# Performance work log

Hardware: AMD Instinct MI355X
Metric: run time of the kernel (lower is better)

Reference implementation:

```python
import jax, jax.numpy as jnp
import numpy as np

NUM_HEADS = 8
CHUNK = 64
TOP_K = 5


def setup_inputs() -> dict:
    key = jax.random.key(0)
    ks = jax.random.split(key, 5)
    D = 512
    x = jax.random.normal(ks[0], (1, 2048, D), dtype=jnp.float32)
    s = 0.02
    Wq = jax.random.normal(ks[1], (D, D), dtype=jnp.float32) * s
    Wk = jax.random.normal(ks[2], (D, D), dtype=jnp.float32) * s
    Wv = jax.random.normal(ks[3], (D, D), dtype=jnp.float32) * s
    Wo = jax.random.normal(ks[4], (D, D), dtype=jnp.float32) * s
    return {"x": x, "Wq": Wq, "Wk": Wk, "Wv": Wv, "Wo": Wo}


def reference(x, Wq, Wk, Wv, Wo):
    B, S, D = x.shape
    H = NUM_HEADS
    hd = D // H
    scale = hd ** -0.5
    C = S // CHUNK  # number of chunks

    def split_heads(t):
        return t.reshape(B, S, H, hd).transpose(0, 2, 1, 3)  # [B,H,S,hd]

    Q = split_heads(x @ Wq)
    K = split_heads(x @ Wk)
    V = split_heads(x @ Wv)

    # chunked K/V: [B,H,C,chunk,hd]
    Kc = K.reshape(B, H, C, CHUNK, hd)
    Vc = V.reshape(B, H, C, CHUNK, hd)

    # chunk descriptors: mean-pooled keys per chunk -> [B,H,C,hd]
    chunk_keys = Kc.mean(axis=3)

    # route each query to top-k chunks by scaled similarity
    sims = jnp.einsum('bhsd,bhcd->bhsc', Q, chunk_keys) * scale  # [B,H,S,C]
    _, idx = jax.lax.top_k(sims, TOP_K)  # [B,H,S,K]

    # gather selected K/V chunk blocks: [B,H,S,K,chunk,hd]
    idx_flat = idx.reshape(B, H, S * TOP_K)[:, :, :, None, None]
    Kg = jnp.take_along_axis(Kc, idx_flat, axis=2).reshape(B, H, S, TOP_K, CHUNK, hd)
    Vg = jnp.take_along_axis(Vc, idx_flat, axis=2).reshape(B, H, S, TOP_K, CHUNK, hd)

    # sparse block attention over the K*chunk gathered keys per query
    scores = jnp.einsum('bhsd,bhskcd->bhskc', Q, Kg) * scale
    attn = jax.nn.softmax(scores.reshape(B, H, S, TOP_K * CHUNK), axis=-1)
    attn = attn.reshape(B, H, S, TOP_K, CHUNK)
    out = jnp.einsum('bhskc,bhskcd->bhsd', attn, Vg)  # [B,H,S,hd]

    out = out.transpose(0, 2, 1, 3).reshape(B, S, D)
    return out @ Wo
```

## Files before the change

kernel.cpp:

```cpp
#include <hip/hip_runtime.h>
#include <hip/hip_bf16.h>
#include <math.h>

#define S_LEN 2048
#define D_DIM 512
#define H_NUM 8
#define HD    64
#define C_NUM 32
#define TOPK  5
#define SCALE 0.125f
#define QCAP  1024
#define ATILES 16

typedef __attribute__((ext_vector_type(8))) short bf16x8;
typedef __attribute__((ext_vector_type(4))) float f32x4;

__device__ __forceinline__ unsigned short f2b(float f) {
    __hip_bfloat16 h = __float2bfloat16(f);
    unsigned short u;
    __builtin_memcpy(&u, &h, 2);
    return u;
}
__device__ __forceinline__ bf16x8 pack8(float4 a, float4 b) {
    bf16x8 r;
    r[0] = (short)f2b(a.x); r[1] = (short)f2b(a.y);
    r[2] = (short)f2b(a.z); r[3] = (short)f2b(a.w);
    r[4] = (short)f2b(b.x); r[5] = (short)f2b(b.y);
    r[6] = (short)f2b(b.z); r[7] = (short)f2b(b.w);
    return r;
}
__device__ __forceinline__ float b2f(unsigned short u) {
    __hip_bfloat16 h;
    __builtin_memcpy(&h, &u, 2);
    return __bfloat162float(h);
}

#define BM 64
#define BN 64
#define BK 32

__device__ __forceinline__ void gemm_body(const float* __restrict__ A,
                                          const float* __restrict__ B,
                                          float* __restrict__ C,
                                          int M, int N, int K,
                                          int bx, int by) {
    __shared__ float As[BK][BM + 4];
    __shared__ float Bs[BK][BN];

    const int t  = threadIdx.x;
    const int tx = t & 15;
    const int ty = t >> 4;
    const int m0 = by * BM;
    const int n0 = bx * BN;

    float4 acc0 = make_float4(0.f,0.f,0.f,0.f);
    float4 acc1 = make_float4(0.f,0.f,0.f,0.f);
    float4 acc2 = make_float4(0.f,0.f,0.f,0.f);
    float4 acc3 = make_float4(0.f,0.f,0.f,0.f);

    const int ar = t >> 3;
    const int ac = (t & 7) * 4;
    const int br = t >> 4;
    const int bc = (t & 15) * 4;

    float4 a0, a1, b0, b1;
    auto LD = [&](int k0) {
        a0 = *(const float4*)&A[(size_t)(m0 + ar)      * K + k0 + ac];
        a1 = *(const float4*)&A[(size_t)(m0 + ar + 32) * K + k0 + ac];
        b0 = *(const float4*)&B[(size_t)(k0 + br)      * N + n0 + bc];
        b1 = *(const float4*)&B[(size_t)(k0 + br + 16) * N + n0 + bc];
    };

    LD(0);
    for (int k0 = 0; k0 < K; k0 += BK) {
        __syncthreads();
        As[ac+0][ar]    = a0.x; As[ac+1][ar]    = a0.y; As[ac+2][ar]    = a0.z; As[ac+3][ar]    = a0.w;
        As[ac+0][ar+32] = a1.x; As[ac+1][ar+32] = a1.y; As[ac+2][ar+32] = a1.z; As[ac+3][ar+32] = a1.w;
        *(float4*)&Bs[br][bc]      = b0;
        *(float4*)&Bs[br + 16][bc] = b1;
        __syncthreads();

        if (k0 + BK < K) LD(k0 + BK);

        #pragma unroll
        for (int kk = 0; kk < BK; ++kk) {
            float4 a = *(const float4*)&As[kk][ty * 4];
            float4 b = *(const float4*)&Bs[kk][tx * 4];
            acc0.x += a.x*b.x; acc0.y += a.x*b.y; acc0.z += a.x*b.z; acc0.w += a.x*b.w;
            acc1.x += a.y*b.x; acc1.y += a.y*b.y; acc1.z += a.y*b.z; acc1.w += a.y*b.w;
            acc2.x += a.z*b.x; acc2.y += a.z*b.y; acc2.z += a.z*b.z; acc2.w += a.z*b.w;
            acc3.x += a.w*b.x; acc3.y += a.w*b.y; acc3.z += a.w*b.z; acc3.w += a.w*b.w;
        }
    }

    *(float4*)&C[(size_t)(m0 + ty*4 + 0) * N + n0 + tx*4] = acc0;
    *(float4*)&C[(size_t)(m0 + ty*4 + 1) * N + n0 + tx*4] = acc1;
    *(float4*)&C[(size_t)(m0 + ty*4 + 2) * N + n0 + tx*4] = acc2;
    *(float4*)&C[(size_t)(m0 + ty*4 + 3) * N + n0 + tx*4] = acc3;
}

__device__ __forceinline__ void gemm_v_body(const float* __restrict__ A,
                                            const float* __restrict__ B,
                                            unsigned short* __restrict__ C,
                                            int M, int N, int K,
                                            int bx, int by) {
    __shared__ unsigned short Asv[64][72];
    __shared__ unsigned short Bsv[64][72];

    const int t  = threadIdx.x;
    const int m0 = by * 64;
    const int n0 = bx * 64;
    const int rl = t >> 2;
    const int c4 = (t & 3) * 16;

    const int lane = t & 63, w = t >> 6, lr = lane & 15, quad = lane >> 4;

    f32x4 acc[4] = {{0.f,0.f,0.f,0.f},{0.f,0.f,0.f,0.f},
                    {0.f,0.f,0.f,0.f},{0.f,0.f,0.f,0.f}};

    float4 fa[4], fb[4];
    auto LDA = [&](int k0) {
        const float* p = &A[(size_t)(m0 + rl) * K + k0 + c4];
        fa[0] = *(const float4*)&p[0];  fa[1] = *(const float4*)&p[4];
        fa[2] = *(const float4*)&p[8];  fa[3] = *(const float4*)&p[12];
    };
    auto LDB = [&](int k0) {
        const float* p = &B[(size_t)(k0 + rl) * N + n0 + c4];
        fb[0] = *(const float4*)&p[0];  fb[1] = *(const float4*)&p[4];
        fb[2] = *(const float4*)&p[8];  fb[3] = *(const float4*)&p[12];
    };

    LDA(0); LDB(0);
    for (int k0 = 0; k0 < K; k0 += 64) {
        __syncthreads();
        *(bf16x8*)&Asv[rl][c4]     = pack8(fa[0], fa[1]);
        *(bf16x8*)&Asv[rl][c4 + 8] = pack8(fa[2], fa[3]);
        #pragma unroll
        for (int f = 0; f < 4; ++f) {
            float4 v = fb[f];
            Bsv[c4 + f*4 + 0][rl] = f2b(v.x);
            Bsv[c4 + f*4 + 1][rl] = f2b(v.y);
            Bsv[c4 + f*4 + 2][rl] = f2b(v.z);
            Bsv[c4 + f*4 + 3][rl] = f2b(v.w);
        }
        __syncthreads();

        if (k0 + 64 < K) { LDA(k0 + 64); LDB(k0 + 64); }

        bf16x8 a0 = *(const bf16x8*)&Asv[w * 16 + lr][quad * 8];
        bf16x8 a1 = *(const bf16x8*)&Asv[w * 16 + lr][32 + quad * 8];
        #pragma unroll
        for (int nt = 0; nt < 4; ++nt) {
            bf16x8 b0 = *(const bf16x8*)&Bsv[nt * 16 + lr][quad * 8];
            bf16x8 b1 = *(const bf16x8*)&Bsv[nt * 16 + lr][32 + quad * 8];
            acc[nt] = __builtin_amdgcn_mfma_f32_16x16x32_bf16(a0, b0, acc[nt], 0, 0, 0);
            acc[nt] = __builtin_amdgcn_mfma_f32_16x16x32_bf16(a1, b1, acc[nt], 0, 0, 0);
        }
    }

    #pragma unroll
    for (int nt = 0; nt < 4; ++nt)
        #pragma unroll
        for (int r = 0; r < 4; ++r) {
            int m = m0 + w * 16 + quad * 4 + r;
            int n = n0 + nt * 16 + lr;
            C[(size_t)m * N + n] = f2b(acc[nt][r]);
        }
}

__global__ __launch_bounds__(256) void gemm_qkvz(const float* __restrict__ x,
                                                 const float* __restrict__ Wq,
                                                 const float* __restrict__ Wk,
                                                 const float* __restrict__ Wv,
                                                 float* __restrict__ Qb,
                                                 float* __restrict__ Kb,
                                                 unsigned short* __restrict__ Vbf,
                                                 int* __restrict__ cur) {
    if (blockIdx.z == 2) {
        if (blockIdx.x == 0 && blockIdx.y == 0) cur[threadIdx.x] = 0;
        gemm_v_body(x, Wv, Vbf, S_LEN, D_DIM, D_DIM, blockIdx.x, blockIdx.y);
    } else {
        const float* B = (blockIdx.z == 0) ? Wq : Wk;
        float*       C = (blockIdx.z == 0) ? Qb : Kb;
        gemm_body(x, B, C, S_LEN, D_DIM, D_DIM, blockIdx.x, blockIdx.y);
    }
}

__global__ __launch_bounds__(256) void chunk_keys_kernel(const float* __restrict__ K,
                                                         float* __restrict__ ck) {
    int i = blockIdx.x * 256 + threadIdx.x;
    int c = i >> 9;
    int d = i & 511;
    const float* p = K + (size_t)c * 64 * D_DIM + d;
    float sum = 0.f;
    #pragma unroll
    for (int r = 0; r < 64; ++r) sum += p[(size_t)r * D_DIM];
    ck[(size_t)c * D_DIM + d] = sum * (1.0f / 64.0f);
}

__global__ __launch_bounds__(256) void sims_topk(const float* __restrict__ Q,
                                                 const float* __restrict__ ck,
                                                 int* __restrict__ cur,
                                                 unsigned short* __restrict__ qlist) {
    __shared__ float qtile[64][68];
    __shared__ float cks[32][68];
    __shared__ float simsb[64][36];
    __shared__ int   lds_cnt[32];
    __shared__ int   lds_base[32];

    const int t  = threadIdx.x;
    const int s0 = blockIdx.x * 64;
    const int h  = blockIdx.y;

    if (t < 32) lds_cnt[t] = 0;

    {
        int r = t >> 2;
        #pragma unroll
        for (int i = 0; i < 4; ++i) {
            int cf4 = (t & 3) * 4 + i;
            *(float4*)&qtile[r][cf4 * 4] =
                *(const float4*)&Q[(size_t)(s0 + r) * D_DIM + h * HD + cf4 * 4];
        }
    }
    for (int i = t; i < C_NUM * 16; i += 256) {
        int c = i >> 4, df4 = i & 15;
        *(float4*)&cks[c][df4 * 4] =
            *(const float4*)&ck[(size_t)c * D_DIM + h * HD + df4 * 4];
    }
    __syncthreads();

    {
        const int sl = t >> 2, g = t & 3;
        float sa[8] = {0.f,0.f,0.f,0.f,0.f,0.f,0.f,0.f};
        #pragma unroll
        for (int d4 = 0; d4 < 16; ++d4) {
            float4 q4 = *(const float4*)&qtile[sl][d4 * 4];
            #pragma unroll
            for (int j = 0; j < 8; ++j) {
                float4 c4 = *(const float4*)&cks[g * 8 + j][d4 * 4];
                sa[j] += q4.x*c4.x + q4.y*c4.y + q4.z*c4.z + q4.w*c4.w;
            }
        }
        *(float4*)&simsb[sl][g*8 + 0] = make_float4(sa[0], sa[1], sa[2], sa[3]);
        *(float4*)&simsb[sl][g*8 + 4] = make_float4(sa[4], sa[5], sa[6], sa[7]);
    }
    __syncthreads();

    int csel[TOPK], lpos[TOPK];
    if (t < 64) {
        float sv[32];
        #pragma unroll
        for (int cq = 0; cq < 8; ++cq) {
            float4 v = *(const float4*)&simsb[t][cq * 4];
            sv[cq*4+0] = v.x; sv[cq*4+1] = v.y; sv[cq*4+2] = v.z; sv[cq*4+3] = v.w;
        }
        #pragma unroll
        for (int k = 0; k < TOPK; ++k) {
            float best = -INFINITY; int bi = 0;
            #pragma unroll
            for (int cc = 0; cc < 32; ++cc) {
                bool gt = sv[cc] > best;
                best = gt ? sv[cc] : best;
                bi   = gt ? cc : bi;
            }
            #pragma unroll
            for (int cc = 0; cc < 32; ++cc)
                if (cc == bi) sv[cc] = -INFINITY;
            csel[k] = bi;
            lpos[k] = atomicAdd(&lds_cnt[bi], 1);
        }
    }
    __syncthreads();

    if (t < 32) lds_base[t] = atomicAdd(&cur[h * 32 + t], lds_cnt[t]);
    __syncthreads();

    if (t < 64) {
        #pragma unroll
        for (int k = 0; k < TOPK; ++k) {
            int c = csel[k];
            int pos = lds_base[c] + lpos[k];
            if (pos < QCAP)
                qlist[(size_t)(h * 32 + c) * QCAP + pos] =
                    (unsigned short)((s0 + t) | (k << 11));
        }
    }
}

__global__ __launch_bounds__(256) void moc_attn6(const float* __restrict__ Q,
                                                 const float* __restrict__ K,
                                                 const unsigned short* __restrict__ Vbf,
                                                 const int* __restrict__ cnt,
                                                 const unsigned short* __restrict__ qlist,
                                                 float* __restrict__ lpart,
                                                 float* __restrict__ Opart) {
    __shared__ unsigned short Qs[64][72];
    __shared__ unsigned short Ks[64][72];
    __shared__ unsigned short VT[64][72];
    __shared__ unsigned short Ps[64][72];
    __shared__ unsigned short slist[64];

    const int hc = blockIdx.y;
    const int h  = hc >> 5;
    const int c  = hc & 31;
    const int g  = blockIdx.x;
    const int t  = threadIdx.x;

    const int count = min(cnt[hc], QCAP);
    const int base  = g * 64;
    if (base >= count) return;
    const int lim = min(count - base, 64);

    const float* Kb = K + ((size_t)c * 64) * D_DIM + h * HD;
    const unsigned short* Vb = Vbf + ((size_t)c * 64) * D_DIM + h * HD;
    const unsigned short* list = qlist + (size_t)hc * QCAP + base;

    {
        const int j  = t >> 2;
        const int d0 = (t & 3) * 16;

        const float* kr = Kb + (size_t)j * D_DIM + d0;
        float4 k0 = *(const float4*)&kr[0],  k1 = *(const float4*)&kr[4];
        float4 k2 = *(const float4*)&kr[8],  k3 = *(const float4*)&kr[12];
        *(bf16x8*)&Ks[j][d0]     = pack8(k0, k1);
        *(bf16x8*)&Ks[j][d0 + 8] = pack8(k2, k3);

        const unsigned short* vr = Vb + (size_t)j * D_DIM + d0;
        bf16x8 v0 = *(const bf16x8*)&vr[0];
        bf16x8 v1 = *(const bf16x8*)&vr[8];
        #pragma unroll
        for (int i = 0; i < 8; ++i) {
            VT[d0 + i][j]     = (unsigned short)v0[i];
            VT[d0 + 8 + i][j] = (unsigned short)v1[i];
        }

        unsigned short pv = (j < lim) ? list[j] : (unsigned short)0xFFFF;
        if ((t & 3) == 0) slist[j] = pv;
        int s = (pv == 0xFFFF) ? 0 : (int)(pv & 2047);
        const float* qr = Q + (size_t)s * D_DIM + h * HD + d0;
        float4 q0 = *(const float4*)&qr[0],  q1 = *(const float4*)&qr[4];
        float4 q2 = *(const float4*)&qr[8],  q3 = *(const float4*)&qr[12];
        *(bf16x8*)&Qs[j][d0]     = pack8(q0, q1);
        *(bf16x8*)&Qs[j][d0 + 8] = pack8(q2, q3);
    }
    __syncthreads();

    const int lane = t & 63;
    const int w    = t >> 6;
    const int lr   = lane & 15;
    const int quad = lane >> 4;

    bf16x8 aq0 = *(const bf16x8*)&Qs[w * 16 + lr][quad * 8];
    bf16x8 aq1 = *(const bf16x8*)&Qs[w * 16 + lr][32 + quad * 8];

    f32x4 acc[4];
    #pragma unroll
    for (int kt = 0; kt < 4; ++kt) {
        bf16x8 b0 = *(const bf16x8*)&Ks[kt * 16 + lr][quad * 8];
        bf16x8 b1 = *(const bf16x8*)&Ks[kt * 16 + lr][32 + quad * 8];
        f32x4 z = {0.f, 0.f, 0.f, 0.f};
        z = __builtin_amdgcn_mfma_f32_16x16x32_bf16(aq0, b0, z, 0, 0, 0);
        z = __builtin_amdgcn_mfma_f32_16x16x32_bf16(aq1, b1, z, 0, 0, 0);
        acc[kt] = z;
    }

    unsigned short pb[4][4];
    float dsum[4] = {0.f, 0.f, 0.f, 0.f};
    #pragma unroll
    for (int kt = 0; kt < 4; ++kt) {
        #pragma unroll
        for (int r = 0; r < 4; ++r) {
            unsigned short u = f2b(__expf(acc[kt][r] * SCALE));
            pb[kt][r] = u;
            dsum[r] += b2f(u);
        }
    }
    #pragma unroll
    for (int r = 0; r < 4; ++r) {
        float v = dsum[r];
        v += __shfl_xor(v, 1, 64);
        v += __shfl_xor(v, 2, 64);
        v += __shfl_xor(v, 4, 64);
        v += __shfl_xor(v, 8, 64);
        dsum[r] = v;
    }
    if (lr == 0) {
        #pragma unroll
        for (int r = 0; r < 4; ++r) {
            unsigned short sv = slist[w * 16 + quad * 4 + r];
            if (sv != 0xFFFF) {
                int kk = sv >> 11, s = sv & 2047;
                lpart[((size_t)kk * H_NUM + h) * S_LEN + s] = dsum[r];
            }
        }
    }

    #pragma unroll
    for (int kt = 0; kt < 4; ++kt)
        #pragma unroll
        for (int r = 0; r < 4; ++r)
            Ps[w * 16 + quad * 4 + r][kt * 16 + lr] = pb[kt][r];

    bf16x8 ap0 = *(const bf16x8*)&Ps[w * 16 + lr][quad * 8];
    bf16x8 ap1 = *(const bf16x8*)&Ps[w * 16 + lr][32 + quad * 8];

    #pragma unroll
    for (int dt = 0; dt < 4; ++dt) {
        bf16x8 b0 = *(const bf16x8*)&VT[dt * 16 + lr][quad * 8];
        bf16x8 b1 = *(const bf16x8*)&VT[dt * 16 + lr][32 + quad * 8];
        f32x4 z = {0.f, 0.f, 0.f, 0.f};
        z = __builtin_amdgcn_mfma_f32_16x16x32_bf16(ap0, b0, z, 0, 0, 0);
        z = __builtin_amdgcn_mfma_f32_16x16x32_bf16(ap1, b1, z, 0, 0, 0);
        #pragma unroll
        for (int r = 0; r < 4; ++r) {
            unsigned short sv = slist[w * 16 + quad * 4 + r];
            if (sv != 0xFFFF) {
                int kk = sv >> 11, s = sv & 2047;
                Opart[((((size_t)kk * H_NUM + h) * S_LEN + s) * HD) + dt * 16 + lr] = z[r];
            }
        }
    }
}

__global__ __launch_bounds__(256) void gemm_out_fused(const float* __restrict__ Opart,
                                                      const float* __restrict__ lpart,
                                                      const float* __restrict__ Wo,
                                                      float* __restrict__ out) {
    __shared__ unsigned short As[64][72];
    __shared__ unsigned short Bs[64][72];

    const int t  = threadIdx.x;
    const int m0 = blockIdx.y * 64;
    const int n0 = blockIdx.x * 64;
    const int rl = t >> 2;
    const int c4 = (t & 3) * 16;

    const int lane = t & 63, w = t >> 6, lr = lane & 15, quad = lane >> 4;
    const int N = D_DIM, K = D_DIM;

    f32x4 acc[4] = {{0.f,0.f,0.f,0.f},{0.f,0.f,0.f,0.f},
                    {0.f,0.f,0.f,0.f},{0.f,0.f,0.f,0.f}};

    float4 fa[4], fb[4];
    auto LDA = [&](int k0) {
        const int kcol = k0 + c4;
        const int h  = kcol >> 6;
        const int d0 = kcol & 63;
        const int m  = m0 + rl;
        fa[0] = make_float4(0.f,0.f,0.f,0.f);
        fa[1] = make_float4(0.f,0.f,0.f,0.f);
        fa[2] = make_float4(0.f,0.f,0.f,0.f);
        fa[3] = make_float4(0.f,0.f,0.f,0.f);
        float den = 0.f;
        #pragma unroll
        for (int r = 0; r < TOPK; ++r) {
            size_t slot = ((size_t)r * H_NUM + h) * S_LEN + m;
            const float* P = Opart + slot * HD + d0;
            float4 v0 = *(const float4*)&P[0],  v1 = *(const float4*)&P[4];
            float4 v2 = *(const float4*)&P[8],  v3 = *(const float4*)&P[12];
            fa[0].x += v0.x; fa[0].y += v0.y; fa[0].z += v0.z; fa[0].w += v0.w;
            fa[1].x += v1.x; fa[1].y += v1.y; fa[1].z += v1.z; fa[1].w += v1.w;
            fa[2].x += v2.x; fa[2].y += v2.y; fa[2].z += v2.z; fa[2].w += v2.w;
            fa[3].x += v3.x; fa[3].y += v3.y; fa[3].z += v3.z; fa[3].w += v3.w;
            den += lpart[slot];
        }
        float inv = 1.0f / den;
        #pragma unroll
        for (int f = 0; f < 4; ++f) {
            fa[f].x *= inv; fa[f].y *= inv; fa[f].z *= inv; fa[f].w *= inv;
        }
    };
    auto LDB = [&](int k0) {
        const float* p = &Wo[(size_t)(k0 + rl) * N + n0 + c4];
        fb[0] = *(const float4*)&p[0];  fb[1] = *(const float4*)&p[4];
        fb[2] = *(const float4*)&p[8];  fb[3] = *(const float4*)&p[12];
    };

    LDA(0); LDB(0);
    for (int k0 = 0; k0 < K; k0 += 64) {
        __syncthreads();
        *(bf16x8*)&As[rl][c4]     = pack8(fa[0], fa[1]);
        *(bf16x8*)&As[rl][c4 + 8] = pack8(fa[2], fa[3]);
        #pragma unroll
        for (int f = 0; f < 4; ++f) {
            float4 v = fb[f];
            Bs[c4 + f*4 + 0][rl] = f2b(v.x);
            Bs[c4 + f*4 + 1][rl] = f2b(v.y);
            Bs[c4 + f*4 + 2][rl] = f2b(v.z);
            Bs[c4 + f*4 + 3][rl] = f2b(v.w);
        }
        __syncthreads();

        if (k0 + 64 < K) { LDA(k0 + 64); LDB(k0 + 64); }

        bf16x8 a0 = *(const bf16x8*)&As[w * 16 + lr][quad * 8];
        bf16x8 a1 = *(const bf16x8*)&As[w * 16 + lr][32 + quad * 8];
        #pragma unroll
        for (int nt = 0; nt < 4; ++nt) {
            bf16x8 b0 = *(const bf16x8*)&Bs[nt * 16 + lr][quad * 8];
            bf16x8 b1 = *(const bf16x8*)&Bs[nt * 16 + lr][32 + quad * 8];
            acc[nt] = __builtin_amdgcn_mfma_f32_16x16x32_bf16(a0, b0, acc[nt], 0, 0, 0);
            acc[nt] = __builtin_amdgcn_mfma_f32_16x16x32_bf16(a1, b1, acc[nt], 0, 0, 0);
        }
    }

    #pragma unroll
    for (int nt = 0; nt < 4; ++nt)
        #pragma unroll
        for (int r = 0; r < 4; ++r) {
            int m = m0 + w * 16 + quad * 4 + r;
            int n = n0 + nt * 16 + lr;
            out[(size_t)m * N + n] = acc[nt][r];
        }
}

extern "C" void kernel_launch(void* const* d_in, const int* in_sizes, int n_in,
                              void* d_out, int out_size, void* d_ws, size_t ws_size,
                              hipStream_t stream) {
    const float* x  = (const float*)d_in[0];
    const float* Wq = (const float*)d_in[1];
    const float* Wk = (const float*)d_in[2];
    const float* Wv = (const float*)d_in[3];
    const float* Wo = (const float*)d_in[4];
    float* out = (float*)d_out;

    const size_t SD = (size_t)S_LEN * D_DIM;
    float* ws    = (float*)d_ws;
    float* Qb    = ws;
    float* Kb    = Qb + SD;
    unsigned short* Vbf = (unsigned short*)(Kb + SD);
    float* ck    = (float*)(Vbf + SD);
    float* lpart = ck + (size_t)C_NUM * D_DIM;
    int*   curb  = (int*)(lpart + (size_t)TOPK * H_NUM * S_LEN);
    unsigned short* qlst = (unsigned short*)(curb + 256);
    float* Opart = (float*)(qlst + (size_t)256 * QCAP);

    dim3 pgrid(D_DIM / 64, S_LEN / 64, 3);
    gemm_qkvz<<<pgrid, 256, 0, stream>>>(x, Wq, Wk, Wv, Qb, Kb, Vbf, curb);

    chunk_keys_kernel<<<(C_NUM * D_DIM) / 256, 256, 0, stream>>>(Kb, ck);

    dim3 rgrid(S_LEN / 64, H_NUM);
    sims_topk<<<rgrid, 256, 0, stream>>>(Qb, ck, curb, qlst);

    dim3 agrid(ATILES, H_NUM * C_NUM);
    moc_attn6<<<agrid, 256, 0, stream>>>(Qb, Kb, Vbf, curb, qlst, lpart, Opart);

    dim3 ogrid(D_DIM / 64, S_LEN / 64);
    gemm_out_fused<<<ogrid, 256, 0, stream>>>(Opart, lpart, Wo, out);
}
```

Baseline: 171.2 us.

## Compute routing sims from x via precomposed Wq·chunk-key matrix and use bf16 Q/K

The routing similarities are computed as x @ G, where G = Wq_h · (mean(x_chunk) @ Wk_h)^T. G is built by new ck and g kernels from chunk-averaged x, so routing no longer depends on Q and K. Q, K and V projections now all run through the MFMA bf16 GEMM and are stored as bf16, which removes fp32 Q/K traffic and the packing work inside attention. The output path is split into a separate reduce/normalize kernel that writes bf16 before a plain MFMA output GEMM. The cost is more kernel launches. Routing sims are now computed in a different order, so near-ties may change which top-k chunks are selected.

```diff
diff --git a/kernel.cpp b/kernel.cpp
--- a/kernel.cpp
+++ b/kernel.cpp
@@ -14,6 +14,7 @@
 
 typedef __attribute__((ext_vector_type(8))) short bf16x8;
 typedef __attribute__((ext_vector_type(4))) float f32x4;
+typedef __attribute__((ext_vector_type(4))) unsigned short us4;
 
 __device__ __forceinline__ unsigned short f2b(float f) {
     __hip_bfloat16 h = __float2bfloat16(f);
@@ -97,6 +98,12 @@
     *(float4*)&C[(size_t)(m0 + ty*4 + 1) * N + n0 + tx*4] = acc1;
     *(float4*)&C[(size_t)(m0 + ty*4 + 2) * N + n0 + tx*4] = acc2;
     *(float4*)&C[(size_t)(m0 + ty*4 + 3) * N + n0 + tx*4] = acc3;
+}
+
+__global__ __launch_bounds__(256) void sims_gemm(const float* __restrict__ x,
+                                                 const float* __restrict__ G,
+                                                 float* __restrict__ sims) {
+    gemm_body(x, G, sims, S_LEN, H_NUM * C_NUM, D_DIM, blockIdx.x, blockIdx.y);
 }
 
 __device__ __forceinline__ void gemm_v_body(const float* __restrict__ A,
@@ -168,42 +175,73 @@
         }
 }
 
-__global__ __launch_bounds__(256) void gemm_qkvz(const float* __restrict__ x,
-                                                 const float* __restrict__ Wq,
+__global__ __launch_bounds__(256) void proj_all(const float* __restrict__ x,
+                                                const float* __restrict__ Wq,
+                                                const float* __restrict__ Wk,
+                                                const float* __restrict__ Wv,
+                                                unsigned short* __restrict__ Qbf,
+                                                unsigned short* __restrict__ Kbf,
+                                                unsigned short* __restrict__ Vbf,
+                                                float* __restrict__ xbar,
+                                                int* __restrict__ cur) {
+    if (blockIdx.z == 3) {
+        int t = threadIdx.x;
+        if (blockIdx.x == 0 && blockIdx.y == 0) cur[t] = 0;
+        int flat = (blockIdx.y * 8 + blockIdx.x) * 256 + t;
+        if (flat < C_NUM * D_DIM) {
+            int c = flat >> 9, d = flat & 511;
+            const float* p = x + (size_t)c * 64 * D_DIM + d;
+            float s = 0.f;
+            #pragma unroll
+            for (int r = 0; r < 64; ++r) s += p[(size_t)r * D_DIM];
+            xbar[flat] = s * (1.0f / 64.0f);
+        }
+        return;
+    }
+    const float* W = (blockIdx.z == 0) ? Wq : (blockIdx.z == 1) ? Wk : Wv;
+    unsigned short* C = (blockIdx.z == 0) ? Qbf : (blockIdx.z == 1) ? Kbf : Vbf;
+    gemm_v_body(x, W, C, S_LEN, D_DIM, D_DIM, blockIdx.x, blockIdx.y);
+}
+
+__global__ __launch_bounds__(256) void ck_kernel(const float* __restrict__ xbar,
                                                  const float* __restrict__ Wk,
-                                                 const float* __restrict__ Wv,
-                                                 float* __restrict__ Qb,
-                                                 float* __restrict__ Kb,
-                                                 unsigned short* __restrict__ Vbf,
-                                                 int* __restrict__ cur) {
-    if (blockIdx.z == 2) {
-        if (blockIdx.x == 0 && blockIdx.y == 0) cur[threadIdx.x] = 0;
-        gemm_v_body(x, Wv, Vbf, S_LEN, D_DIM, D_DIM, blockIdx.x, blockIdx.y);
-    } else {
-        const float* B = (blockIdx.z == 0) ? Wq : Wk;
-        float*       C = (blockIdx.z == 0) ? Qb : Kb;
-        gemm_body(x, B, C, S_LEN, D_DIM, D_DIM, blockIdx.x, blockIdx.y);
-    }
-}
-
-__global__ __launch_bounds__(256) void chunk_keys_kernel(const float* __restrict__ K,
-                                                         float* __restrict__ ck) {
-    int i = blockIdx.x * 256 + threadIdx.x;
-    int c = i >> 9;
-    int d = i & 511;
-    const float* p = K + (size_t)c * 64 * D_DIM + d;
-    float sum = 0.f;
-    #pragma unroll
-    for (int r = 0; r < 64; ++r) sum += p[(size_t)r * D_DIM];
-    ck[(size_t)c * D_DIM + d] = sum * (1.0f / 64.0f);
-}
-
-__global__ __launch_bounds__(256) void sims_topk(const float* __restrict__ Q,
-                                                 const float* __restrict__ ck,
-                                                 int* __restrict__ cur,
-                                                 unsigned short* __restrict__ qlist) {
-    __shared__ float qtile[64][68];
-    __shared__ float cks[32][68];
+                                                 float* __restrict__ ck) {
+    __shared__ float xl[512];
+    const int c = blockIdx.x, t = threadIdx.x;
+    xl[t]       = xbar[c * 512 + t];
+    xl[t + 256] = xbar[c * 512 + t + 256];
+    __syncthreads();
+    float s0 = 0.f, s1 = 0.f;
+    #pragma unroll 8
+    for (int j = 0; j < 512; ++j) {
+        float xv = xl[j];
+        s0 += xv * Wk[(size_t)j * 512 + t];
+        s1 += xv * Wk[(size_t)j * 512 + t + 256];
+    }
+    ck[c * 512 + t]       = s0;
+    ck[c * 512 + t + 256] = s1;
+}
+
+__global__ __launch_bounds__(256) void g_kernel(const float* __restrict__ Wq,
+                                                const float* __restrict__ ck,
+                                                float* __restrict__ G) {
+    __shared__ float ckl[32][513];
+    __shared__ float wql[512];
+    const int j = blockIdx.x, t = threadIdx.x;
+    for (int i = t; i < 32 * 512; i += 256) ckl[i >> 9][i & 511] = ck[i];
+    wql[t]       = Wq[(size_t)j * 512 + t];
+    wql[t + 256] = Wq[(size_t)j * 512 + t + 256];
+    __syncthreads();
+    const int h = t >> 5, c = t & 31;
+    float s = 0.f;
+    #pragma unroll
+    for (int d = 0; d < 64; ++d) s += wql[h * 64 + d] * ckl[c][h * 64 + d];
+    G[(size_t)j * 256 + t] = s;
+}
+
+__global__ __launch_bounds__(256) void topk_scatter(const float* __restrict__ sims,
+                                                    int* __restrict__ cur,
+                                                    unsigned short* __restrict__ qlist) {
     __shared__ float simsb[64][36];
     __shared__ int   lds_cnt[32];
     __shared__ int   lds_base[32];
@@ -213,37 +251,11 @@
     const int h  = blockIdx.y;
 
     if (t < 32) lds_cnt[t] = 0;
-
     {
-        int r = t >> 2;
-        #pragma unroll
-        for (int i = 0; i < 4; ++i) {
-            int cf4 = (t & 3) * 4 + i;
-            *(float4*)&qtile[r][cf4 * 4] =
-                *(const float4*)&Q[(size_t)(s0 + r) * D_DIM + h * HD + cf4 * 4];
-        }
-    }
-    for (int i = t; i < C_NUM * 16; i += 256) {
-        int c = i >> 4, df4 = i & 15;
-        *(float4*)&cks[c][df4 * 4] =
-            *(const float4*)&ck[(size_t)c * D_DIM + h * HD + df4 * 4];
-    }
-    __syncthreads();
-
-    {
-        const int sl = t >> 2, g = t & 3;
-        float sa[8] = {0.f,0.f,0.f,0.f,0.f,0.f,0.f,0.f};
-        #pragma unroll
-        for (int d4 = 0; d4 < 16; ++d4) {
-            float4 q4 = *(const float4*)&qtile[sl][d4 * 4];
-            #pragma unroll
-            for (int j = 0; j < 8; ++j) {
-                float4 c4 = *(const float4*)&cks[g * 8 + j][d4 * 4];
-                sa[j] += q4.x*c4.x + q4.y*c4.y + q4.z*c4.z + q4.w*c4.w;
-            }
-        }
-        *(float4*)&simsb[sl][g*8 + 0] = make_float4(sa[0], sa[1], sa[2], sa[3]);
-        *(float4*)&simsb[sl][g*8 + 4] = make_float4(sa[4], sa[5], sa[6], sa[7]);
+        int r = t >> 2, cg = (t & 3) * 8;
+        const float* sp = sims + (size_t)(s0 + r) * 256 + h * 32 + cg;
+        *(float4*)&simsb[r][cg]     = *(const float4*)&sp[0];
+        *(float4*)&simsb[r][cg + 4] = *(const float4*)&sp[4];
     }
     __syncthreads();
 
@@ -288,13 +300,13 @@
     }
 }
 
-__global__ __launch_bounds__(256) void moc_attn6(const float* __restrict__ Q,
-                                                 const float* __restrict__ K,
-                                                 const unsigned short* __restrict__ Vbf,
-                                                 const int* __restrict__ cnt,
-                                                 const unsigned short* __restrict__ qlist,
-                                                 float* __restrict__ lpart,
-                                                 float* __restrict__ Opart) {
+__global__ __launch_bounds__(256) void moc_attn6b(const unsigned short* __restrict__ Qbf,
+                                                  const unsigned short* __restrict__ Kbf,
+                                                  const unsigned short* __restrict__ Vbf,
+                                                  const int* __restrict__ cnt,
+                                                  const unsigned short* __restrict__ qlist,
+                                                  float* __restrict__ lpart,
+                                                  float* __restrict__ Opart) {
     __shared__ unsigned short Qs[64][72];
     __shared__ unsigned short Ks[64][72];
     __shared__ unsigned short VT[64][72];
@@ -312,7 +324,7 @@
     if (base >= count) return;
     const int lim = min(count - base, 64);
 
-    const float* Kb = K + ((size_t)c * 64) * D_DIM + h * HD;
+    const unsigned short* Kb = Kbf + ((size_t)c * 64) * D_DIM + h * HD;
     const unsigned short* Vb = Vbf + ((size_t)c * 64) * D_DIM + h * HD;
     const unsigned short* list = qlist + (size_t)hc * QCAP + base;
 
@@ -320,11 +332,9 @@
         const int j  = t >> 2;
         const int d0 = (t & 3) * 16;
 
-        const float* kr = Kb + (size_t)j * D_DIM + d0;
-        float4 k0 = *(const float4*)&kr[0],  k1 = *(const float4*)&kr[4];
-        float4 k2 = *(const float4*)&kr[8],  k3 = *(const float4*)&kr[12];
-        *(bf16x8*)&Ks[j][d0]     = pack8(k0, k1);
-        *(bf16x8*)&Ks[j][d0 + 8] = pack8(k2, k3);
+        const unsigned short* kr = Kb + (size_t)j * D_DIM + d0;
+        *(bf16x8*)&Ks[j][d0]     = *(const bf16x8*)&kr[0];
+        *(bf16x8*)&Ks[j][d0 + 8] = *(const bf16x8*)&kr[8];
 
         const unsigned short* vr = Vb + (size_t)j * D_DIM + d0;
         bf16x8 v0 = *(const bf16x8*)&vr[0];
@@ -338,11 +348,9 @@
         unsigned short pv = (j < lim) ? list[j] : (unsigned short)0xFFFF;
         if ((t & 3) == 0) slist[j] = pv;
         int s = (pv == 0xFFFF) ? 0 : (int)(pv & 2047);
-        const float* qr = Q + (size_t)s * D_DIM + h * HD + d0;
-        float4 q0 = *(const float4*)&qr[0],  q1 = *(const float4*)&qr[4];
-        float4 q2 = *(const float4*)&qr[8],  q3 = *(const float4*)&qr[12];
-        *(bf16x8*)&Qs[j][d0]     = pack8(q0, q1);
-        *(bf16x8*)&Qs[j][d0 + 8] = pack8(q2, q3);
+        const unsigned short* qr = Qbf + (size_t)s * D_DIM + h * HD + d0;
+        *(bf16x8*)&Qs[j][d0]     = *(const bf16x8*)&qr[0];
+        *(bf16x8*)&Qs[j][d0 + 8] = *(const bf16x8*)&qr[8];
     }
     __syncthreads();
 
@@ -423,10 +431,33 @@
     }
 }
 
-__global__ __launch_bounds__(256) void gemm_out_fused(const float* __restrict__ Opart,
-                                                      const float* __restrict__ lpart,
-                                                      const float* __restrict__ Wo,
-                                                      float* __restrict__ out) {
+__global__ __launch_bounds__(256) void reduce_norm(const float4* __restrict__ Opart4,
+                                                   const float* __restrict__ lpart,
+                                                   unsigned short* __restrict__ Obn) {
+    int i = blockIdx.x * 256 + threadIdx.x;
+    int s    = i >> 7;
+    int col4 = i & 127;
+    int h    = col4 >> 4;
+    int f4   = col4 & 15;
+    float4 acc = make_float4(0.f,0.f,0.f,0.f);
+    float  den = 0.f;
+    #pragma unroll
+    for (int k = 0; k < TOPK; ++k) {
+        size_t slot = ((size_t)k * H_NUM + h) * S_LEN + s;
+        float4 v = Opart4[slot * 16 + f4];
+        acc.x += v.x; acc.y += v.y; acc.z += v.z; acc.w += v.w;
+        den += lpart[slot];
+    }
+    float inv = 1.0f / den;
+    us4 o;
+    o[0] = f2b(acc.x * inv); o[1] = f2b(acc.y * inv);
+    o[2] = f2b(acc.z * inv); o[3] = f2b(acc.w * inv);
+    *(us4*)&Obn[(size_t)i * 4] = o;
+}
+
+__global__ __launch_bounds__(256) void gemm_out(const unsigned short* __restrict__ Obn,
+                                                const float* __restrict__ Wo,
+                                                float* __restrict__ out) {
     __shared__ unsigned short As[64][72];
     __shared__ unsigned short Bs[64][72];
 
@@ -435,41 +466,18 @@
     const int n0 = blockIdx.x * 64;
     const int rl = t >> 2;
     const int c4 = (t & 3) * 16;
+    const int N = D_DIM, K = D_DIM;
 
     const int lane = t & 63, w = t >> 6, lr = lane & 15, quad = lane >> 4;
-    const int N = D_DIM, K = D_DIM;
 
     f32x4 acc[4] = {{0.f,0.f,0.f,0.f},{0.f,0.f,0.f,0.f},
                     {0.f,0.f,0.f,0.f},{0.f,0.f,0.f,0.f}};
 
-    float4 fa[4], fb[4];
+    bf16x8 ba[2]; float4 fb[4];
     auto LDA = [&](int k0) {
-        const int kcol = k0 + c4;
-        const int h  = kcol >> 6;
-        const int d0 = kcol & 63;
-        const int m  = m0 + rl;
-        fa[0] = make_float4(0.f,0.f,0.f,0.f);
-        fa[1] = make_float4(0.f,0.f,0.f,0.f);
-        fa[2] = make_float4(0.f,0.f,0.f,0.f);
-        fa[3] = make_float4(0.f,0.f,0.f,0.f);
-        float den = 0.f;
-        #pragma unroll
-        for (int r = 0; r < TOPK; ++r) {
-            size_t slot = ((size_t)r * H_NUM + h) * S_LEN + m;
-            const float* P = Opart + slot * HD + d0;
-            float4 v0 = *(const float4*)&P[0],  v1 = *(const float4*)&P[4];
-            float4 v2 = *(const float4*)&P[8],  v3 = *(const float4*)&P[12];
-            fa[0].x += v0.x; fa[0].y += v0.y; fa[0].z += v0.z; fa[0].w += v0.w;
-            fa[1].x += v1.x; fa[1].y += v1.y; fa[1].z += v1.z; fa[1].w += v1.w;
-            fa[2].x += v2.x; fa[2].y += v2.y; fa[2].z += v2.z; fa[2].w += v2.w;
-            fa[3].x += v3.x; fa[3].y += v3.y; fa[3].z += v3.z; fa[3].w += v3.w;
-            den += lpart[slot];
-        }
-        float inv = 1.0f / den;
-        #pragma unroll
-        for (int f = 0; f < 4; ++f) {
-            fa[f].x *= inv; fa[f].y *= inv; fa[f].z *= inv; fa[f].w *= inv;
-        }
+        const unsigned short* p = &Obn[(size_t)(m0 + rl) * K + k0 + c4];
+        ba[0] = *(const bf16x8*)&p[0];
+        ba[1] = *(const bf16x8*)&p[8];
     };
     auto LDB = [&](int k0) {
         const float* p = &Wo[(size_t)(k0 + rl) * N + n0 + c4];
@@ -480,8 +488,8 @@
     LDA(0); LDB(0);
     for (int k0 = 0; k0 < K; k0 += 64) {
         __syncthreads();
-        *(bf16x8*)&As[rl][c4]     = pack8(fa[0], fa[1]);
-        *(bf16x8*)&As[rl][c4 + 8] = pack8(fa[2], fa[3]);
+        *(bf16x8*)&As[rl][c4]     = ba[0];
+        *(bf16x8*)&As[rl][c4 + 8] = ba[1];
         #pragma unroll
         for (int f = 0; f < 4; ++f) {
             float4 v = fb[f];
@@ -526,27 +534,37 @@
     float* out = (float*)d_out;
 
     const size_t SD = (size_t)S_LEN * D_DIM;
-    float* ws    = (float*)d_ws;
-    float* Qb    = ws;
-    float* Kb    = Qb + SD;
-    unsigned short* Vbf = (unsigned short*)(Kb + SD);
-    float* ck    = (float*)(Vbf + SD);
-    float* lpart = ck + (size_t)C_NUM * D_DIM;
+    unsigned short* Qbf = (unsigned short*)d_ws;
+    unsigned short* Kbf = Qbf + SD;
+    unsigned short* Vbf = Kbf + SD;
+    float* xbar = (float*)(Vbf + SD);
+    float* ck   = xbar + (size_t)C_NUM * D_DIM;
+    float* G    = ck + (size_t)C_NUM * D_DIM;
+    float* sims = G + (size_t)D_DIM * (H_NUM * C_NUM);
+    float* lpart = sims + (size_t)S_LEN * (H_NUM * C_NUM);
     int*   curb  = (int*)(lpart + (size_t)TOPK * H_NUM * S_LEN);
     unsigned short* qlst = (unsigned short*)(curb + 256);
     float* Opart = (float*)(qlst + (size_t)256 * QCAP);
-
-    dim3 pgrid(D_DIM / 64, S_LEN / 64, 3);
-    gemm_qkvz<<<pgrid, 256, 0, stream>>>(x, Wq, Wk, Wv, Qb, Kb, Vbf, curb);
-
-    chunk_keys_kernel<<<(C_NUM * D_DIM) / 256, 256, 0, stream>>>(Kb, ck);
+    unsigned short* Obn = (unsigned short*)sims;
+
+    dim3 pgrid(D_DIM / 64, S_LEN / 64, 4);
+    proj_all<<<pgrid, 256, 0, stream>>>(x, Wq, Wk, Wv, Qbf, Kbf, Vbf, xbar, curb);
+
+    ck_kernel<<<C_NUM, 256, 0, stream>>>(xbar, Wk, ck);
+
+    g_kernel<<<D_DIM, 256, 0, stream>>>(Wq, ck, G);
+
+    dim3 sgrid((H_NUM * C_NUM) / BN, S_LEN / BM);
+    sims_gemm<<<sgrid, 256, 0, stream>>>(x, G, sims);
 
     dim3 rgrid(S_LEN / 64, H_NUM);
-    sims_topk<<<rgrid, 256, 0, stream>>>(Qb, ck, curb, qlst);
+    topk_scatter<<<rgrid, 256, 0, stream>>>(sims, curb, qlst);
 
     dim3 agrid(ATILES, H_NUM * C_NUM);
-    moc_attn6<<<agrid, 256, 0, stream>>>(Qb, Kb, Vbf, curb, qlst, lpart, Opart);
+    moc_attn6b<<<agrid, 256, 0, stream>>>(Qbf, Kbf, Vbf, curb, qlst, lpart, Opart);
+
+    reduce_norm<<<(int)(SD / 4 / 256), 256, 0, stream>>>((const float4*)Opart, lpart, Obn);
 
     dim3 ogrid(D_DIM / 64, S_LEN / 64);
-    gemm_out_fused<<<ogrid, 256, 0, stream>>>(Opart, lpart, Wo, out);
-}
+    gemm_out<<<ogrid, 256, 0, stream>>>(Obn, Wo, out);
+}
```

Result: slower. 181.8 us (+6.2%).
